# Performance work log

Hardware: AMD Instinct MI355X
Metric: run time of the kernel (lower is better)

The kernel has to match this reference:

```python
import jax, jax.numpy as jnp
import numpy as np

BN_EPS = 1e-5
N_NODES = 100000
N_EDGES = 300000
IN_FEAT = 256
HIDDEN = 128
N_ETYPES = 4


def setup_inputs() -> dict:
    key = jax.random.key(0)
    ks = jax.random.split(key, 10)
    s = 1.0 / np.sqrt(2 * IN_FEAT)
    return {
        "h_src": jax.random.normal(ks[0], (N_NODES, IN_FEAT), jnp.float32),
        "h_dst": jax.random.normal(ks[1], (N_NODES, IN_FEAT), jnp.float32),
        "src_nodes": jax.random.randint(ks[2], (N_EDGES,), 0, N_NODES),
        "dst_nodes": jax.random.randint(ks[3], (N_EDGES,), 0, N_NODES),
        "etype_idx": 0,
        "W1": jax.random.normal(ks[4], (2 * IN_FEAT, HIDDEN), jnp.float32) * s,
        "b1": jnp.zeros((HIDDEN,), jnp.float32),
        "bn_gamma": jnp.ones((HIDDEN,), jnp.float32),
        "bn_beta": jnp.zeros((HIDDEN,), jnp.float32),
        "bn_mean": jnp.zeros((HIDDEN,), jnp.float32),
        "bn_var": jnp.ones((HIDDEN,), jnp.float32),
        "emb": jax.random.normal(ks[5], (N_ETYPES, HIDDEN), jnp.float32),
        "W2": jax.random.normal(ks[6], (HIDDEN, HIDDEN // 2), jnp.float32) * (1.0 / np.sqrt(HIDDEN)),
        "b2": jnp.zeros((HIDDEN // 2,), jnp.float32),
        "W3": jax.random.normal(ks[7], (HIDDEN // 2, 1), jnp.float32) * (1.0 / np.sqrt(HIDDEN // 2)),
        "b3": jnp.zeros((1,), jnp.float32),
    }


def reference(h_src, h_dst, src_nodes, dst_nodes, etype_idx,
              W1, b1, bn_gamma, bn_beta, bn_mean, bn_var,
              emb, W2, b2, W3, b3):
    # gather endpoint features and concat -> [E, 2*in_feat]
    src_feat = h_src[src_nodes]
    dst_feat = h_dst[dst_nodes]
    edge_feat = jnp.concatenate([src_feat, dst_feat], axis=1)
    # Linear + ReLU (Dropout is identity in eval) + BatchNorm1d (running stats)
    x = jax.nn.relu(edge_feat @ W1 + b1)
    x = (x - bn_mean) * jax.lax.rsqrt(bn_var + BN_EPS) * bn_gamma + bn_beta
    # add edge-type embedding (broadcast over edges)
    x = x + emb[etype_idx]
    # per-edge-type predictor MLP -> scalar score per edge
    x = jax.nn.relu(x @ W2 + b2)
    scores = (x @ W3 + b3).squeeze(-1)
    return scores
```

## Files before the change

kernel.cpp:

```cpp
#include <hip/hip_runtime.h>
#include <hip/hip_bf16.h>


typedef __attribute__((ext_vector_type(8))) short bf16x8;
typedef __attribute__((ext_vector_type(4))) float f32x4;
typedef __attribute__((ext_vector_type(8))) unsigned short u16x8;

constexpr int HID   = 128;
constexpr int ETILE = 64;
constexpr int AS    = 72;
constexpr int XS    = 136;

__device__ inline ushort f2bf(float f) {
    union { __hip_bfloat16 h; ushort u; } cv;
    cv.h = __float2bfloat16(f);
    return cv.u;
}
__device__ inline float bf2f(ushort u) {
    return __uint_as_float(((unsigned int)u) << 16);
}

__global__ __launch_bounds__(256)
void prep_kernel(const float* __restrict__ W1, const float* __restrict__ W2,
                 const float* __restrict__ bn_gamma, const float* __restrict__ bn_beta,
                 const float* __restrict__ bn_mean, const float* __restrict__ bn_var,
                 const float* __restrict__ emb, const int* __restrict__ etype,
                 ushort* __restrict__ B1p, ushort* __restrict__ B2p,
                 float* __restrict__ sc, float* __restrict__ sh)
{
    int i = blockIdx.x * blockDim.x + threadIdx.x;
    if (i < 65536) {
        int j = i & 7, lane = (i >> 3) & 63, ct = (i >> 9) & 7, ks = i >> 12;
        int k = ks * 32 + (lane >> 4) * 8 + j;
        int c = ct * 16 + (lane & 15);
        B1p[i] = f2bf(W1[k * HID + c]);
    } else if (i < 65536 + 8192) {
        int p = i - 65536;
        int j = p & 7, lane = (p >> 3) & 63, ct = (p >> 9) & 3, ks = p >> 11;
        int k = ks * 32 + (lane >> 4) * 8 + j;
        int c = ct * 16 + (lane & 15);
        B2p[p] = f2bf(W2[k * 64 + c]);
    } else if (i < 65536 + 8192 + HID) {
        int c = i - 65536 - 8192;
        float s = bn_gamma[c] * rsqrtf(bn_var[c] + 1e-5f);
        sc[c] = s;
        sh[c] = bn_beta[c] - bn_mean[c] * s + emb[etype[0] * HID + c];
    }
}

__global__ __launch_bounds__(256)
void proj_kernel(const float* __restrict__ h_src, const float* __restrict__ h_dst,
                 const ushort* __restrict__ B1p, const float* __restrict__ b1,
                 ushort* __restrict__ Psrc, ushort* __restrict__ Pdst,
                 int n_nodes, int ntiles)
{
    __shared__ ushort sA[ETILE * XS];

    const int t    = threadIdx.x;
    const int lane = t & 63;
    const int w    = t >> 6;
    const int lr   = lane & 15;
    const int lq   = lane >> 4;

#pragma unroll 1
    for (int half = 0; half < 2; ++half) {
        const float* hp = half ? h_dst : h_src;
        ushort* Pp      = half ? Pdst : Psrc;
        const int nb    = blockIdx.x * 64;

        f32x4 acc[4][2];
#pragma unroll
        for (int rt = 0; rt < 4; ++rt)
#pragma unroll
            for (int c = 0; c < 2; ++c) acc[rt][c] = (f32x4)0.0f;

        for (int kc = 0; kc < 2; ++kc) {
            const int koff = kc * 128;
            __syncthreads();

#pragma unroll
            for (int i = 0; i < 8; ++i) {
                int f = t + i * 256;
                int e = f >> 5, q = f & 31;
                int row = nb + e;
                if (row >= n_nodes) row = n_nodes - 1;
                float4 v = *reinterpret_cast<const float4*>(
                    hp + (size_t)row * 256 + koff + q * 4);
                ushort4 bv;
                bv.x = f2bf(v.x); bv.y = f2bf(v.y); bv.z = f2bf(v.z); bv.w = f2bf(v.w);
                *reinterpret_cast<ushort4*>(&sA[e * XS + q * 4]) = bv;
            }
            __syncthreads();

#pragma unroll
            for (int ks = 0; ks < 4; ++ks) {
                const int kstep = half * 8 + kc * 4 + ks;
                bf16x8 bf0 = *reinterpret_cast<const bf16x8*>(
                    B1p + (size_t)((kstep * 8 + 2 * w) * 64 + lane) * 8);
                bf16x8 bf1 = *reinterpret_cast<const bf16x8*>(
                    B1p + (size_t)((kstep * 8 + 2 * w + 1) * 64 + lane) * 8);
#pragma unroll
                for (int rt = 0; rt < 4; ++rt) {
                    bf16x8 af = *reinterpret_cast<const bf16x8*>(
                        &sA[(rt * 16 + lr) * XS + ks * 32 + lq * 8]);
                    acc[rt][0] = __builtin_amdgcn_mfma_f32_16x16x32_bf16(af, bf0, acc[rt][0], 0, 0, 0);
                    acc[rt][1] = __builtin_amdgcn_mfma_f32_16x16x32_bf16(af, bf1, acc[rt][1], 0, 0, 0);
                }
            }
        }

        __syncthreads();

#pragma unroll
        for (int ctl = 0; ctl < 2; ++ctl) {
            int c = (2 * w + ctl) * 16 + lr;
            float add = half ? b1[c] : 0.0f;
#pragma unroll
            for (int rt = 0; rt < 4; ++rt)
#pragma unroll
                for (int r = 0; r < 4; ++r)
                    sA[(rt * 16 + lq * 4 + r) * XS + c] = f2bf(acc[rt][ctl][r] + add);
        }
        __syncthreads();

#pragma unroll
        for (int i = 0; i < 4; ++i) {
            int f = t + i * 256;
            int e = f >> 4, q = f & 15;
            if (nb + e < n_nodes) {
                u16x8 v = *reinterpret_cast<const u16x8*>(&sA[e * XS + q * 8]);
                *reinterpret_cast<u16x8*>(Pp + (size_t)(nb + e) * 128 + q * 8) = v;
            }
        }
    }
}

__global__ __launch_bounds__(256)
void edge_kernel(const ushort* __restrict__ Psrc, const ushort* __restrict__ Pdst,
                 const int* __restrict__ src_nodes, const int* __restrict__ dst_nodes,
                 const float* __restrict__ sc, const float* __restrict__ sh,
                 const float* __restrict__ b2, const float* __restrict__ W3,
                 const float* __restrict__ b3, const ushort* __restrict__ B2p,
                 float* __restrict__ out, int n_edges)
{
    __shared__ ushort sX[ETILE * XS];
    __shared__ int s_s[ETILE], s_d[ETILE];

    const int t     = threadIdx.x;
    const int lane  = t & 63;
    const int w     = t >> 6;
    const int lr    = lane & 15;
    const int lq    = lane >> 4;
    const int ebase = blockIdx.x * ETILE;

    if (t < ETILE) {
        int e = ebase + t;
        s_s[t] = src_nodes[e < n_edges ? e : (n_edges - 1)];
    } else if (t < 2 * ETILE) {
        int e = ebase + t - ETILE;
        s_d[t - ETILE] = dst_nodes[e < n_edges ? e : (n_edges - 1)];
    }
    __syncthreads();

    const int eg = w * 16 + lq;
    const int ch = lr;
    u16x8 gs[4], gd[4];
#pragma unroll
    for (int j = 0; j < 4; ++j)
        gs[j] = *reinterpret_cast<const u16x8*>(
            Psrc + (size_t)s_s[eg + j * 4] * 128 + ch * 8);
#pragma unroll
    for (int j = 0; j < 4; ++j)
        gd[j] = *reinterpret_cast<const u16x8*>(
            Pdst + (size_t)s_d[eg + j * 4] * 128 + ch * 8);
    asm volatile("" :: "v"(gs[0]), "v"(gs[1]), "v"(gs[2]), "v"(gs[3]),
                       "v"(gd[0]), "v"(gd[1]), "v"(gd[2]), "v"(gd[3]));

    const int c0 = ch * 8;
    float4 sca = *reinterpret_cast<const float4*>(sc + c0);
    float4 scb = *reinterpret_cast<const float4*>(sc + c0 + 4);
    float4 sha = *reinterpret_cast<const float4*>(sh + c0);
    float4 shb = *reinterpret_cast<const float4*>(sh + c0 + 4);
    float ss[8] = {sca.x, sca.y, sca.z, sca.w, scb.x, scb.y, scb.z, scb.w};
    float zz[8] = {sha.x, sha.y, sha.z, sha.w, shb.x, shb.y, shb.z, shb.w};
#pragma unroll
    for (int j = 0; j < 4; ++j) {
        u16x8 xo;
#pragma unroll
        for (int i = 0; i < 8; ++i) {
            float v = bf2f((ushort)gs[j][i]) + bf2f((ushort)gd[j][i]);
            v = fmaxf(v, 0.0f);
            xo[i] = f2bf(fmaf(v, ss[i], zz[i]));
        }
        *reinterpret_cast<u16x8*>(&sX[(eg + j * 4) * XS + c0]) = xo;
    }
    __syncthreads();

    f32x4 acc2[4];
#pragma unroll
    for (int ct = 0; ct < 4; ++ct) acc2[ct] = (f32x4)0.0f;

#pragma unroll
    for (int ks = 0; ks < 4; ++ks) {
        bf16x8 af = *reinterpret_cast<const bf16x8*>(
            &sX[(w * 16 + lr) * XS + ks * 32 + lq * 8]);
#pragma unroll
        for (int ct = 0; ct < 4; ++ct) {
            bf16x8 bf = *reinterpret_cast<const bf16x8*>(
                B2p + (size_t)((ks * 4 + ct) * 64 + lane) * 8);
            acc2[ct] = __builtin_amdgcn_mfma_f32_16x16x32_bf16(af, bf, acc2[ct], 0, 0, 0);
        }
    }

    float w3v[4], b2v[4];
#pragma unroll
    for (int ct = 0; ct < 4; ++ct) {
        int c = ct * 16 + lr;
        w3v[ct] = W3[c];
        b2v[ct] = b2[c];
    }
#pragma unroll
    for (int r = 0; r < 4; ++r) {
        float sum = 0.0f;
#pragma unroll
        for (int ct = 0; ct < 4; ++ct)
            sum += fmaxf(acc2[ct][r] + b2v[ct], 0.0f) * w3v[ct];
        sum += __shfl_xor(sum, 1);
        sum += __shfl_xor(sum, 2);
        sum += __shfl_xor(sum, 4);
        sum += __shfl_xor(sum, 8);
        int eo = ebase + w * 16 + lq * 4 + r;
        if (lr == 0 && eo < n_edges) out[eo] = sum + b3[0];
    }
}

__global__ __launch_bounds__(256, 3)
void edge_mlp_mfma(const float* __restrict__ h_src, const float* __restrict__ h_dst,
                   const int* __restrict__ src_nodes, const int* __restrict__ dst_nodes,
                   const ushort* __restrict__ B1p, const ushort* __restrict__ B2p,
                   const float* __restrict__ b1, const float* __restrict__ sc,
                   const float* __restrict__ sh, const float* __restrict__ b2,
                   const float* __restrict__ W3, const float* __restrict__ b3,
                   float* __restrict__ out, int n_edges)
{
    __shared__ ushort sA[2][ETILE * AS];
    __shared__ int s_src[ETILE], s_dst[ETILE];

    const int t    = threadIdx.x;
    const int lane = t & 63;
    const int w    = t >> 6;
    const int lr   = lane & 15;
    const int lq   = lane >> 4;
    const int ebase = blockIdx.x * ETILE;

    if (t < ETILE) {
        int e = ebase + t;
        s_src[t] = src_nodes[e < n_edges ? e : 0];
    } else if (t < 2 * ETILE) {
        int e = ebase + t - ETILE;
        s_dst[t - ETILE] = dst_nodes[e < n_edges ? e : 0];
    }

    f32x4 acc[4][2];
#pragma unroll
    for (int rt = 0; rt < 4; ++rt)
#pragma unroll
        for (int c = 0; c < 2; ++c) acc[rt][c] = (f32x4)0.0f;

    float4 rA[4], rB[4];
    bf16x8 Bf0[4], Bf1[4];

#define PHASE_BAR() do {                                                       \
        asm volatile("s_waitcnt lgkmcnt(0)" ::: "memory");                     \
        __builtin_amdgcn_s_barrier();                                          \
    } while (0)
#define PIN() __builtin_amdgcn_sched_barrier(0)

#define LOADC(kc, R) do {                                                      \
        const float* hp = ((kc) < 4) ? h_src : h_dst;                          \
        const int* sidx = ((kc) < 4) ? s_src : s_dst;                          \
        const int koff = ((kc) & 3) * 64;                                      \
        _Pragma("unroll")                                                      \
        for (int i = 0; i < 4; ++i) {                                          \
            int f = t + i * 256; int e = f >> 4; int q = f & 15;               \
            R[i] = *reinterpret_cast<const float4*>(                           \
                hp + (size_t)sidx[e] * 256 + koff + q * 4);                    \
        } } while (0)

#define BLOAD(kc, BR) do {                                                     \
        _Pragma("unroll")                                                      \
        for (int s = 0; s < 2; ++s)                                            \
        _Pragma("unroll")                                                      \
        for (int c = 0; c < 2; ++c)                                            \
            BR[s * 2 + c] = *reinterpret_cast<const bf16x8*>(                  \
                B1p + (size_t)((((kc) * 2 + s) * 8 + 2 * w + c) * 64 + lane) * 8); \
        } while (0)

#define STOREC(B, R) do {                                                      \
        _Pragma("unroll")                                                      \
        for (int i = 0; i < 4; ++i) {                                          \
            int f = t + i * 256; int e = f >> 4; int q = f & 15;               \
            ushort4 bv;                                                        \
            bv.x = f2bf(R[i].x); bv.y = f2bf(R[i].y);                          \
            bv.z = f2bf(R[i].z); bv.w = f2bf(R[i].w);                          \
            *reinterpret_cast<ushort4*>(&sA[B][e * AS + q * 4]) = bv;          \
        } } while (0)

#define COMPF(B, BR) do {                                                      \
        _Pragma("unroll")                                                      \
        for (int ks = 0; ks < 2; ++ks) {                                       \
            _Pragma("unroll")                                                  \
            for (int rt = 0; rt < 4; ++rt) {                                   \
                bf16x8 af = *reinterpret_cast<const bf16x8*>(                  \
                    &sA[B][(rt * 16 + lr) * AS + ks * 32 + lq * 8]);           \
                acc[rt][0] = __builtin_amdgcn_mfma_f32_16x16x32_bf16(af, BR[ks * 2 + 0], acc[rt][0], 0, 0, 0); \
                acc[rt][1] = __builtin_amdgcn_mfma_f32_16x16x32_bf16(af, BR[ks * 2 + 1], acc[rt][1], 0, 0, 0); \
            } } } while (0)

    __syncthreads();

    LOADC(0, rA);
    BLOAD(0, Bf0);
    STOREC(0, rA);
    LOADC(1, rB);
    BLOAD(1, Bf1);
    PHASE_BAR();

    LOADC(2, rA);  PIN();  COMPF(0, Bf0);  BLOAD(2, Bf0);  STOREC(1, rB);  PHASE_BAR();
    LOADC(3, rB);  PIN();  COMPF(1, Bf1);  BLOAD(3, Bf1);  STOREC(0, rA);  PHASE_BAR();
    LOADC(4, rA);  PIN();  COMPF(0, Bf0);  BLOAD(4, Bf0);  STOREC(1, rB);  PHASE_BAR();
    LOADC(5, rB);  PIN();  COMPF(1, Bf1);  BLOAD(5, Bf1);  STOREC(0, rA);  PHASE_BAR();
    LOADC(6, rA);  PIN();  COMPF(0, Bf0);  BLOAD(6, Bf0);  STOREC(1, rB);  PHASE_BAR();
    LOADC(7, rB);  PIN();  COMPF(1, Bf1);  BLOAD(7, Bf1);  STOREC(0, rA);  PHASE_BAR();
                           COMPF(0, Bf0);                  STOREC(1, rB);  PHASE_BAR();
                           COMPF(1, Bf1);

#undef LOADC
#undef BLOAD
#undef STOREC
#undef COMPF
#undef PIN
#undef PHASE_BAR

    __syncthreads();
    ushort* sX = &sA[0][0];
#pragma unroll
    for (int ctl = 0; ctl < 2; ++ctl) {
        int c = (2 * w + ctl) * 16 + lr;
        float bb = b1[c], s = sc[c], z = sh[c];
#pragma unroll
        for (int rt = 0; rt < 4; ++rt)
#pragma unroll
            for (int r = 0; r < 4; ++r) {
                float x = fmaxf(acc[rt][ctl][r] + bb, 0.0f);
                sX[(rt * 16 + lq * 4 + r) * XS + c] = f2bf(fmaf(x, s, z));
            }
    }
    __syncthreads();

    f32x4 acc2[4];
#pragma unroll
    for (int ct = 0; ct < 4; ++ct) acc2[ct] = (f32x4)0.0f;

#pragma unroll
    for (int ks = 0; ks < 4; ++ks) {
        bf16x8 af = *reinterpret_cast<const bf16x8*>(
            &sX[(w * 16 + lr) * XS + ks * 32 + lq * 8]);
#pragma unroll
        for (int ct = 0; ct < 4; ++ct) {
            bf16x8 bf = *reinterpret_cast<const bf16x8*>(
                B2p + (size_t)((ks * 4 + ct) * 64 + lane) * 8);
            acc2[ct] = __builtin_amdgcn_mfma_f32_16x16x32_bf16(af, bf, acc2[ct], 0, 0, 0);
        }
    }

    float w3v[4], b2v[4];
#pragma unroll
    for (int ct = 0; ct < 4; ++ct) {
        int c = ct * 16 + lr;
        w3v[ct] = W3[c];
        b2v[ct] = b2[c];
    }
#pragma unroll
    for (int r = 0; r < 4; ++r) {
        float sum = 0.0f;
#pragma unroll
        for (int ct = 0; ct < 4; ++ct)
            sum += fmaxf(acc2[ct][r] + b2v[ct], 0.0f) * w3v[ct];
        sum += __shfl_xor(sum, 1);
        sum += __shfl_xor(sum, 2);
        sum += __shfl_xor(sum, 4);
        sum += __shfl_xor(sum, 8);
        int e = ebase + w * 16 + lq * 4 + r;
        if (lr == 0 && e < n_edges) out[e] = sum + b3[0];
    }
}

extern "C" void kernel_launch(void* const* d_in, const int* in_sizes, int n_in,
                              void* d_out, int out_size, void* d_ws, size_t ws_size,
                              hipStream_t stream) {
    const float* h_src     = (const float*)d_in[0];
    const float* h_dst     = (const float*)d_in[1];
    const int*   src_nodes = (const int*)d_in[2];
    const int*   dst_nodes = (const int*)d_in[3];
    const int*   etype     = (const int*)d_in[4];
    const float* W1        = (const float*)d_in[5];
    const float* b1        = (const float*)d_in[6];
    const float* bn_gamma  = (const float*)d_in[7];
    const float* bn_beta   = (const float*)d_in[8];
    const float* bn_mean   = (const float*)d_in[9];
    const float* bn_var    = (const float*)d_in[10];
    const float* emb       = (const float*)d_in[11];
    const float* W2        = (const float*)d_in[12];
    const float* b2        = (const float*)d_in[13];
    const float* W3        = (const float*)d_in[14];
    const float* b3        = (const float*)d_in[15];

    const int n_edges = in_sizes[2];
    const int n_nodes = in_sizes[0] / 256;

    ushort* B1p = (ushort*)d_ws;
    ushort* B2p = B1p + 65536;
    float*  scp = (float*)(B2p + 8192);
    float*  shp = scp + HID;
    const size_t wbytes = (size_t)(65536 + 8192) * 2 + 256 * 4;
    const size_t pbytes = (size_t)n_nodes * HID * 2;
    ushort* Psrc = (ushort*)((char*)d_ws + wbytes);
    ushort* Pdst = Psrc + (size_t)n_nodes * HID;

    prep_kernel<<<(65536 + 8192 + HID + 255) / 256, 256, 0, stream>>>(
        W1, W2, bn_gamma, bn_beta, bn_mean, bn_var, emb, etype, B1p, B2p, scp, shp);

    const int egrid = (n_edges + ETILE - 1) / ETILE;

    if (ws_size >= wbytes + 2 * pbytes) {
        const int ntiles = (n_nodes + 63) / 64;
        proj_kernel<<<ntiles, 256, 0, stream>>>(h_src, h_dst, B1p, b1,
                                                Psrc, Pdst, n_nodes, ntiles);
        edge_kernel<<<egrid, 256, 0, stream>>>(Psrc, Pdst, src_nodes, dst_nodes,
                                               scp, shp, b2, W3, b3, B2p,
                                               (float*)d_out, n_edges);
    } else {
        edge_mlp_mfma<<<egrid, 256, 0, stream>>>(h_src, h_dst, src_nodes, dst_nodes,
                                                 B1p, B2p, b1, scp, shp, b2, W3, b3,
                                                 (float*)d_out, n_edges);
    }
}
```

Measured before the change: 92.37 us.

## Make proj kernel persistent with register-resident W1 fragments and full-K staging

The projection kernel now runs a grid-stride loop over node tiles with about a third as many blocks. Each wave loads its W1 B-fragments for all 8 k-steps into registers once per half, instead of re-reading them from global memory per tile. It also stages the full 256-wide input row into a larger LDS tile, which cuts the K-chunk loop and its barriers. The trade is much higher register pressure (16 bf16x8 fragments plus accumulators) and double the LDS footprint, which can reduce occupancy for this memory-bound kernel.

```diff
diff --git a/kernel.cpp b/kernel.cpp
--- a/kernel.cpp
+++ b/kernel.cpp
@@ -10,6 +10,7 @@
 constexpr int ETILE = 64;
 constexpr int AS    = 72;
 constexpr int XS    = 136;
+constexpr int PS    = 264;
 
 __device__ inline ushort f2bf(float f) {
     union { __hip_bfloat16 h; ushort u; } cv;
@@ -52,9 +53,9 @@
 void proj_kernel(const float* __restrict__ h_src, const float* __restrict__ h_dst,
                  const ushort* __restrict__ B1p, const float* __restrict__ b1,
                  ushort* __restrict__ Psrc, ushort* __restrict__ Pdst,
-                 int n_nodes, int ntiles)
+                 int n_nodes, int ntiles, int nblk)
 {
-    __shared__ ushort sA[ETILE * XS];
+    __shared__ ushort sA[ETILE * PS];
 
     const int t    = threadIdx.x;
     const int lane = t & 63;
@@ -66,70 +67,73 @@
     for (int half = 0; half < 2; ++half) {
         const float* hp = half ? h_dst : h_src;
         ushort* Pp      = half ? Pdst : Psrc;
-        const int nb    = blockIdx.x * 64;
-
-        f32x4 acc[4][2];
-#pragma unroll
-        for (int rt = 0; rt < 4; ++rt)
-#pragma unroll
-            for (int c = 0; c < 2; ++c) acc[rt][c] = (f32x4)0.0f;
-
-        for (int kc = 0; kc < 2; ++kc) {
-            const int koff = kc * 128;
+
+        bf16x8 bfr[8][2];
+#pragma unroll
+        for (int ks = 0; ks < 8; ++ks)
+#pragma unroll
+            for (int ctl = 0; ctl < 2; ++ctl)
+                bfr[ks][ctl] = *reinterpret_cast<const bf16x8*>(
+                    B1p + (size_t)(((half * 8 + ks) * 8 + 2 * w + ctl) * 64 + lane) * 8);
+
+#pragma unroll 1
+        for (int tile = blockIdx.x; tile < ntiles; tile += nblk) {
+            const int nb = tile * 64;
+
             __syncthreads();
 
 #pragma unroll
-            for (int i = 0; i < 8; ++i) {
+            for (int i = 0; i < 16; ++i) {
                 int f = t + i * 256;
-                int e = f >> 5, q = f & 31;
+                int e = f >> 6, q = f & 63;
                 int row = nb + e;
                 if (row >= n_nodes) row = n_nodes - 1;
                 float4 v = *reinterpret_cast<const float4*>(
-                    hp + (size_t)row * 256 + koff + q * 4);
+                    hp + (size_t)row * 256 + q * 4);
                 ushort4 bv;
                 bv.x = f2bf(v.x); bv.y = f2bf(v.y); bv.z = f2bf(v.z); bv.w = f2bf(v.w);
-                *reinterpret_cast<ushort4*>(&sA[e * XS + q * 4]) = bv;
+                *reinterpret_cast<ushort4*>(&sA[e * PS + q * 4]) = bv;
             }
             __syncthreads();
 
-#pragma unroll
-            for (int ks = 0; ks < 4; ++ks) {
-                const int kstep = half * 8 + kc * 4 + ks;
-                bf16x8 bf0 = *reinterpret_cast<const bf16x8*>(
-                    B1p + (size_t)((kstep * 8 + 2 * w) * 64 + lane) * 8);
-                bf16x8 bf1 = *reinterpret_cast<const bf16x8*>(
-                    B1p + (size_t)((kstep * 8 + 2 * w + 1) * 64 + lane) * 8);
+            f32x4 acc[4][2];
+#pragma unroll
+            for (int rt = 0; rt < 4; ++rt)
+#pragma unroll
+                for (int c = 0; c < 2; ++c) acc[rt][c] = (f32x4)0.0f;
+
+#pragma unroll
+            for (int ks = 0; ks < 8; ++ks)
 #pragma unroll
                 for (int rt = 0; rt < 4; ++rt) {
                     bf16x8 af = *reinterpret_cast<const bf16x8*>(
-                        &sA[(rt * 16 + lr) * XS + ks * 32 + lq * 8]);
-                    acc[rt][0] = __builtin_amdgcn_mfma_f32_16x16x32_bf16(af, bf0, acc[rt][0], 0, 0, 0);
-                    acc[rt][1] = __builtin_amdgcn_mfma_f32_16x16x32_bf16(af, bf1, acc[rt][1], 0, 0, 0);
+                        &sA[(rt * 16 + lr) * PS + ks * 32 + lq * 8]);
+                    acc[rt][0] = __builtin_amdgcn_mfma_f32_16x16x32_bf16(af, bfr[ks][0], acc[rt][0], 0, 0, 0);
+                    acc[rt][1] = __builtin_amdgcn_mfma_f32_16x16x32_bf16(af, bfr[ks][1], acc[rt][1], 0, 0, 0);
                 }
+
+            __syncthreads();
+
+#pragma unroll
+            for (int ctl = 0; ctl < 2; ++ctl) {
+                int c = (2 * w + ctl) * 16 + lr;
+                float add = half ? b1[c] : 0.0f;
+#pragma unroll
+                for (int rt = 0; rt < 4; ++rt)
+#pragma unroll
+                    for (int r = 0; r < 4; ++r)
+                        sA[(rt * 16 + lq * 4 + r) * PS + c] = f2bf(acc[rt][ctl][r] + add);
             }
-        }
-
-        __syncthreads();
-
-#pragma unroll
-        for (int ctl = 0; ctl < 2; ++ctl) {
-            int c = (2 * w + ctl) * 16 + lr;
-            float add = half ? b1[c] : 0.0f;
-#pragma unroll
-            for (int rt = 0; rt < 4; ++rt)
-#pragma unroll
-                for (int r = 0; r < 4; ++r)
-                    sA[(rt * 16 + lq * 4 + r) * XS + c] = f2bf(acc[rt][ctl][r] + add);
-        }
-        __syncthreads();
-
-#pragma unroll
-        for (int i = 0; i < 4; ++i) {
-            int f = t + i * 256;
-            int e = f >> 4, q = f & 15;
-            if (nb + e < n_nodes) {
-                u16x8 v = *reinterpret_cast<const u16x8*>(&sA[e * XS + q * 8]);
-                *reinterpret_cast<u16x8*>(Pp + (size_t)(nb + e) * 128 + q * 8) = v;
+            __syncthreads();
+
+#pragma unroll
+            for (int i = 0; i < 4; ++i) {
+                int f = t + i * 256;
+                int e = f >> 4, q = f & 15;
+                if (nb + e < n_nodes) {
+                    u16x8 v = *reinterpret_cast<const u16x8*>(&sA[e * PS + q * 8]);
+                    *reinterpret_cast<u16x8*>(Pp + (size_t)(nb + e) * 128 + q * 8) = v;
+                }
             }
         }
     }
@@ -435,8 +439,9 @@
 
     if (ws_size >= wbytes + 2 * pbytes) {
         const int ntiles = (n_nodes + 63) / 64;
-        proj_kernel<<<ntiles, 256, 0, stream>>>(h_src, h_dst, B1p, b1,
-                                                Psrc, Pdst, n_nodes, ntiles);
+        const int nblk   = (ntiles + 2) / 3;
+        proj_kernel<<<nblk, 256, 0, stream>>>(h_src, h_dst, B1p, b1,
+                                              Psrc, Pdst, n_nodes, ntiles, nblk);
         edge_kernel<<<egrid, 256, 0, stream>>>(Psrc, Pdst, src_nodes, dst_nodes,
                                                scp, shp, b2, W3, b3, B2p,
                                                (float*)d_out, n_edges);
```

After: 87.25 us, median of 2. 1.06x faster.
